# Kernel optimization log

Measured on AMD Instinct MI355X. Metric: run time of the kernel, lower is better.

## Reference

```python
import jax, jax.numpy as jnp
import numpy as np

DIST_THRESH = 2.0
YAW_THRESH = np.pi / 3
PI = np.pi


def setup_inputs() -> dict:
    key = jax.random.key(0)
    k1, k2, k3 = jax.random.split(key, 3)
    B, K, T = 32, 16, 30
    N, n = 128, 20
    preds = jax.random.normal(k1, (B, K, T, 2), dtype=jnp.float32)
    centerline_nodes = jax.random.normal(k2, (B, N, n, 2), dtype=jnp.float32)
    centerline_node_masks = jax.random.randint(k3, (B, N, n), 0, 2, dtype=jnp.int32)
    return {
        "preds": preds,
        "centerline_nodes": centerline_nodes,
        "centerline_node_masks": centerline_node_masks,
    }


def _yaw_from_traj(traj):
    # traj: (..., L, 2) -> yaw (..., L), first element zero
    dv = traj[..., 1:, :] - traj[..., :-1, :]
    yaw = -jnp.arctan2(dv[..., 0], dv[..., 1])
    zeros = jnp.zeros(yaw.shape[:-1] + (1,), dtype=yaw.dtype)
    return jnp.concatenate([zeros, yaw], axis=-1)


def reference(preds, centerline_nodes, centerline_node_masks):
    B, K, T, _ = preds.shape
    pred_yaw = _yaw_from_traj(preds)                  # (B, K, T)
    node_yaw = _yaw_from_traj(centerline_nodes)       # (B, N, n)

    cn = centerline_nodes.reshape(B, -1, 2)           # (B, Nn, 2)
    mask = centerline_node_masks.reshape(B, -1)       # (B, Nn)
    pts = preds.reshape(B, -1, 2)                     # (B, KT, 2)

    # pairwise euclidean distance via ||a||^2 + ||b||^2 - 2 a.b
    a2 = jnp.sum(cn * cn, axis=-1)                    # (B, Nn)
    b2 = jnp.sum(pts * pts, axis=-1)                  # (B, KT)
    d2 = a2[:, :, None] + b2[:, None, :] - 2.0 * jnp.einsum("bnd,bkd->bnk", cn, pts)
    dists = jnp.sqrt(jnp.maximum(d2, 0.0))            # (B, Nn, KT)
    dists = jnp.where((mask == 1)[:, :, None], jnp.inf, dists)

    yaw_diffs = node_yaw.reshape(B, -1)[:, :, None] - pred_yaw.reshape(B, -1)[:, None, :]
    yaw_diffs = (yaw_diffs + PI) % (2.0 * PI) - PI    # wrap to [-pi, pi)

    cost = jax.nn.relu(dists - DIST_THRESH) + jax.nn.relu(jnp.abs(yaw_diffs) - YAW_THRESH)
    consistency = jnp.min(cost, axis=1)               # (B, KT)
    return consistency.reshape(B, K, T).sum(axis=-1)  # (B, K)
```

## Files before the change

### kernel.cpp

```cpp
#include <hip/hip_runtime.h>
#include <math.h>

#define B_     32
#define K_     16
#define T_     30
#define KT_    480
#define N_     128
#define NPN_   20
#define NODES_ 2560
#define CH_    32
#define CSZ_   80

#define PI_F      3.14159265358979323846f
#define TWO_PI_F  6.28318530717958647692f
#define YAW_TH_F  (PI_F / 3.0f)


__global__ __launch_bounds__(256) void cm_main(
    const float* __restrict__ preds,
    const float* __restrict__ cn,
    const int*   __restrict__ cmask,
    float*       __restrict__ ws_part)
{
  const int b   = blockIdx.x >> 5;
  const int c   = blockIdx.x & (CH_ - 1);
  const int tid = threadIdx.x;

  __shared__ float4 nd[CSZ_ + 8];
  __shared__ int    s_cnt;

  if (tid == 0) s_cnt = 0;
  __syncthreads();

  if (tid < CSZ_) {
    const int gn = c * CSZ_ + tid;
    const int mv = cmask[(size_t)b * NODES_ + gn];
    if (mv != 1) {
      const int j = gn % NPN_;
      const float2* cnb = (const float2*)cn + (size_t)b * NODES_;
      const float2 p = cnb[gn];
      float yaw = 0.0f;
      if (j != 0) {
        const float2 q = cnb[gn - 1];
        yaw = -atan2f(p.x - q.x, p.y - q.y);
      }
      const float a2 = fmaf(p.x, p.x, p.y * p.y);
      const int pos = atomicAdd(&s_cnt, 1);
      nd[pos] = make_float4(-2.0f * p.x, -2.0f * p.y, a2, yaw);
    }
  }

  const int kt0 = tid;
  const int kt1 = tid + 256;
  const float2* pb = (const float2*)preds + (size_t)b * KT_;
  float4 p0, p1;
  {
    const float2 pp = pb[kt0];
    float pyaw = 0.0f;
    if ((kt0 % T_) != 0) {
      const float2 pq = pb[kt0 - 1];
      pyaw = -atan2f(pp.x - pq.x, pp.y - pq.y);
    }
    p0 = make_float4(pp.x, pp.y, fmaf(pp.x, pp.x, pp.y * pp.y), pyaw);
  }
  if (kt1 < KT_) {
    const float2 pp = pb[kt1];
    float pyaw = 0.0f;
    if ((kt1 % T_) != 0) {
      const float2 pq = pb[kt1 - 1];
      pyaw = -atan2f(pp.x - pq.x, pp.y - pq.y);
    }
    p1 = make_float4(pp.x, pp.y, fmaf(pp.x, pp.x, pp.y * pp.y), pyaw);
  } else {
    p1 = make_float4(0.f, 0.f, 0.f, 0.f);
  }

  __syncthreads();
  const int cnt  = s_cnt;
  const int npad = (cnt + 7) & ~7;
  if (tid < npad - cnt)
    nd[cnt + tid] = make_float4(0.f, 0.f, INFINITY, 0.f);
  __syncthreads();

  float m0 = INFINITY, m1 = INFINITY;
  for (int i = 0; i < npad; i += 8) {
    #pragma unroll
    for (int j = 0; j < 8; ++j) {
      const float4 nv = nd[i + j];
      {
        float t = nv.z + p0.z;
        t = fmaf(nv.x, p0.x, t);
        t = fmaf(nv.y, p0.y, t);
        t = fmaxf(t, 4.0f);
        const float s  = __builtin_amdgcn_sqrtf(t);
        const float yd = nv.w - p0.w;
        const float a  = fminf(fabsf(yd), TWO_PI_F - fabsf(yd));
        const float yc = fmaxf(a - YAW_TH_F, 0.0f);
        m0 = fminf(m0, s + yc);
      }
      {
        float t = nv.z + p1.z;
        t = fmaf(nv.x, p1.x, t);
        t = fmaf(nv.y, p1.y, t);
        t = fmaxf(t, 4.0f);
        const float s  = __builtin_amdgcn_sqrtf(t);
        const float yd = nv.w - p1.w;
        const float a  = fminf(fabsf(yd), TWO_PI_F - fabsf(yd));
        const float yc = fmaxf(a - YAW_TH_F, 0.0f);
        m1 = fminf(m1, s + yc);
      }
    }
  }

  float* wp = ws_part + ((size_t)b * CH_ + c) * KT_;
  wp[kt0] = m0;
  if (kt1 < KT_) wp[kt1] = m1;
}

__global__ __launch_bounds__(512) void cm_reduce(
    const float* __restrict__ ws_part, float* __restrict__ out)
{
  const int b   = blockIdx.x;
  const int tid = threadIdx.x;
  __shared__ float sc[KT_];

  if (tid < KT_) {
    const float* wp = ws_part + (size_t)b * CH_ * KT_;
    float m = INFINITY;
    #pragma unroll
    for (int c = 0; c < CH_; ++c) m = fminf(m, wp[c * KT_ + tid]);
    sc[tid] = m - 2.0f;
  }
  __syncthreads();

  if (tid < K_) {
    float s = 0.0f;
    #pragma unroll
    for (int t = 0; t < T_; ++t) s += sc[tid * T_ + t];
    out[b * K_ + tid] = s;
  }
}

extern "C" void kernel_launch(void* const* d_in, const int* in_sizes, int n_in,
                              void* d_out, int out_size, void* d_ws, size_t ws_size,
                              hipStream_t stream) {
  const float* preds = (const float*)d_in[0];
  const float* cn    = (const float*)d_in[1];
  const int*   cmask = (const int*)d_in[2];
  float* out = (float*)d_out;
  float* ws_part = (float*)d_ws;

  cm_main<<<dim3(B_ * CH_), dim3(256), 0, stream>>>(preds, cn, cmask, ws_part);
  cm_reduce<<<dim3(B_), dim3(512), 0, stream>>>(ws_part, out);
}
```

Baseline: 69.17 us.

## Track min squared distance with yaw gating and exit early when cost is zero

The inner loop now keeps the minimum squared distance over yaw-compatible nodes, with no sqrt, and breaks out once every lane in the wavefront has found a zero-cost node. If any lane has not reached zero cost, a full exact pass recomputes the true minimum cost. This aims to cut ALU and sqrt work for typical inputs where zero-cost matches are common. The cost is a second full pass whenever any lane in a wavefront is unsatisfied.

```diff
diff --git a/kernel.cpp b/kernel.cpp
--- a/kernel.cpp
+++ b/kernel.cpp
@@ -82,7 +82,8 @@
     nd[cnt + tid] = make_float4(0.f, 0.f, INFINITY, 0.f);
   __syncthreads();
 
-  float m0 = INFINITY, m1 = INFINITY;
+  float md2_0 = INFINITY;
+  float md2_1 = (kt1 < KT_) ? INFINITY : 0.0f;
   for (int i = 0; i < npad; i += 8) {
     #pragma unroll
     for (int j = 0; j < 8; ++j) {
@@ -91,25 +92,50 @@
         float t = nv.z + p0.z;
         t = fmaf(nv.x, p0.x, t);
         t = fmaf(nv.y, p0.y, t);
-        t = fmaxf(t, 4.0f);
-        const float s  = __builtin_amdgcn_sqrtf(t);
         const float yd = nv.w - p0.w;
         const float a  = fminf(fabsf(yd), TWO_PI_F - fabsf(yd));
-        const float yc = fmaxf(a - YAW_TH_F, 0.0f);
-        m0 = fminf(m0, s + yc);
+        md2_0 = fminf(md2_0, (a <= YAW_TH_F) ? t : INFINITY);
       }
       {
         float t = nv.z + p1.z;
         t = fmaf(nv.x, p1.x, t);
         t = fmaf(nv.y, p1.y, t);
-        t = fmaxf(t, 4.0f);
-        const float s  = __builtin_amdgcn_sqrtf(t);
         const float yd = nv.w - p1.w;
         const float a  = fminf(fabsf(yd), TWO_PI_F - fabsf(yd));
-        const float yc = fmaxf(a - YAW_TH_F, 0.0f);
-        m1 = fminf(m1, s + yc);
+        md2_1 = fminf(md2_1, (a <= YAW_TH_F) ? t : INFINITY);
       }
     }
+    if (__all((md2_0 <= 4.0f) && (md2_1 <= 4.0f))) break;
+  }
+
+  float m0 = __builtin_amdgcn_sqrtf(fmaxf(md2_0, 4.0f));
+  float m1 = __builtin_amdgcn_sqrtf(fmaxf(md2_1, 4.0f));
+
+  if (__any((md2_0 > 4.0f) || (md2_1 > 4.0f))) {
+    float f0 = INFINITY, f1 = INFINITY;
+    for (int i = 0; i < npad; ++i) {
+      const float4 nv = nd[i];
+      {
+        float t = nv.z + p0.z;
+        t = fmaf(nv.x, p0.x, t);
+        t = fmaf(nv.y, p0.y, t);
+        const float s  = __builtin_amdgcn_sqrtf(fmaxf(t, 4.0f));
+        const float yd = nv.w - p0.w;
+        const float a  = fminf(fabsf(yd), TWO_PI_F - fabsf(yd));
+        f0 = fminf(f0, s + fmaxf(a - YAW_TH_F, 0.0f));
+      }
+      {
+        float t = nv.z + p1.z;
+        t = fmaf(nv.x, p1.x, t);
+        t = fmaf(nv.y, p1.y, t);
+        const float s  = __builtin_amdgcn_sqrtf(fmaxf(t, 4.0f));
+        const float yd = nv.w - p1.w;
+        const float a  = fminf(fabsf(yd), TWO_PI_F - fabsf(yd));
+        f1 = fminf(f1, s + fmaxf(a - YAW_TH_F, 0.0f));
+      }
+    }
+    m0 = fminf(m0, f0);
+    m1 = fminf(m1, f1);
   }
 
   float* wp = ws_part + ((size_t)b * CH_ + c) * KT_;
```

Measured after the change: 72.23 us. 4.4% more time.
